# Kernel optimization log

Hardware: AMD Instinct MI355X
Metric: run time of the kernel (lower is better)

The kernel has to match this reference:

```python
import jax, jax.numpy as jnp
import numpy as np

# Finance / model constants (from Hyperparams)
S0 = 1.0
MU = 0.0
VOL = 0.2
TEXP = 5.0
PRINCIPAL = 100.0
LAM = 0.01
DT = 1.0 / 12.0
N_STEPS = 60            # texp / dt
GMDB = 100.0            # gmdb_frac * principal
FEE = 0.0196            # stand-in for analytics.calc_fair_fee(...)
BATCH = 65536
HIDDEN = 128
W_STD = 0.05
B_STD = 0.05


def setup_inputs() -> dict:
    key = jax.random.key(0)
    ks = jax.random.split(key, 8)
    # GBM paths: spots[i, j] = spot at time index i on path j, shape [N_STEPS+1, BATCH]
    z = jax.random.normal(ks[0], (N_STEPS, BATCH), dtype=jnp.float32)
    logret = (MU - 0.5 * VOL * VOL) * DT + VOL * np.sqrt(DT).astype(np.float32) * z
    spots = S0 * jnp.exp(jnp.concatenate([jnp.zeros((1, BATCH), jnp.float32),
                                          jnp.cumsum(logret, axis=0)], axis=0))
    tn = lambda k, shape, std: (jax.random.truncated_normal(k, -2.0, 2.0, shape, jnp.float32) * std)
    return {
        "spots": spots,
        "W1": tn(ks[1], (2, HIDDEN), W_STD),
        "b1": tn(ks[2], (HIDDEN,), B_STD),
        "W2": tn(ks[3], (HIDDEN, HIDDEN), W_STD),
        "b2": tn(ks[4], (HIDDEN,), B_STD),
        "W3": tn(ks[5], (HIDDEN, 1), W_STD),
        "b3": tn(ks[6], (1,), B_STD),
    }


def _hedge_delta(x, W1, b1, W2, b2, W3, b3):
    # 2-hidden-layer ReLU MLP -> 1 output; hedge delta = -(net(x))^2
    h = jax.nn.relu(x @ W1 + b1)
    h = jax.nn.relu(h @ W2 + b2)
    out = h @ W3 + b3          # [B, 1]
    return -(out ** 2)[:, 0]   # [B]


def reference(spots, W1, b1, W2, b2, W3, b3):
    """compute_pnl: returns per-path integrated PNL, shape [BATCH]."""
    ts = jnp.arange(N_STEPS, dtype=spots.dtype) * DT  # [N_STEPS]

    def step(pnl, xs):
        spot, spot_next, t = xs  # spot: [B]
        inputs = jnp.stack([spot, spot * 0 + t], axis=1)  # [B, 2]
        delta = _hedge_delta(inputs, W1, b1, W2, b2, W3, b3)
        delta = delta * jnp.minimum(jnp.exp(-0.01 * delta), 1.0)
        delta = delta * ((1.0 - jnp.exp(-LAM * (TEXP - t))) * PRINCIPAL)
        account = PRINCIPAL * spot / S0 * jnp.exp(-FEE * t)
        fee = FEE * DT * account * jnp.exp(-LAM * t)
        payout = LAM * DT * jnp.maximum(GMDB - account, 0.0) * jnp.exp(-LAM * t)
        inc_pnl = fee - payout
        pnl = pnl + inc_pnl + delta * (spot_next - spot)
        return pnl, None

    pnl0 = jnp.zeros(spots.shape[1], dtype=spots.dtype)
    pnl, _ = jax.lax.scan(step, pnl0, (spots[:-1], spots[1:], ts))
    return pnl
```

## Files before the change

### kernel.cpp

```cpp
#include <hip/hip_runtime.h>
#include <math.h>

namespace {
constexpr int kBatch = 65536;
constexpr int kSteps = 60;
constexpr int kNodes = 256;
constexpr float kInvDx = 16.0f;
constexpr float kDx    = 1.0f / 16.0f;

constexpr int kTPS   = kNodes / 16;
constexpr int kTiles = kSteps * kTPS;
constexpr int kBuildBlocks = 480;

constexpr float kDT        = 1.0f / 12.0f;
constexpr float kLam       = 0.01f;
constexpr float kTexp      = 5.0f;
constexpr float kPrincipal = 100.0f;
constexpr float kGmdb      = 100.0f;
constexpr float kFee       = 0.0196f;
}

typedef short short8 __attribute__((ext_vector_type(8)));
typedef float f32x4  __attribute__((ext_vector_type(4)));

__device__ inline short f2bf(float f) {
    unsigned u = __builtin_bit_cast(unsigned, f);
    u += 0x7FFFu + ((u >> 16) & 1u);
    return (short)(u >> 16);
}

__device__ inline unsigned short f2h_bits(float f) {
    return __builtin_bit_cast(unsigned short, (_Float16)f);
}
__device__ inline float h2f(unsigned short h) {
    return (float)__builtin_bit_cast(_Float16, h);
}

__global__ __launch_bounds__(256) void va_build_table(
    const float* __restrict__ W1,
    const float* __restrict__ b1,
    const float* __restrict__ W2,
    const float* __restrict__ b2,
    const float* __restrict__ W3,
    const float* __restrict__ b3,
    unsigned* __restrict__ tabu)
{
    const int tid   = threadIdx.x;
    const int lane  = tid & 63;
    const int lo    = lane & 15;
    const int hi    = lane >> 4;
    const int wv    = tid >> 6;
    const int mslot = wv >> 1;
    const int nh    = wv & 1;

    short8 bfrag[4][4];
    float  b2v[4], w3v[4];
    #pragma unroll
    for (int nt = 0; nt < 4; ++nt) {
        const int col = nh * 64 + nt * 16 + lo;
        b2v[nt] = b2[col];
        w3v[nt] = W3[col];
        #pragma unroll
        for (int kc = 0; kc < 4; ++kc) {
            const int kb = kc * 32 + hi * 8;
            short8 bf;
            #pragma unroll
            for (int e = 0; e < 8; ++e)
                bf[e] = f2bf(W2[(kb + e) * 128 + col]);
            bfrag[nt][kc] = bf;
        }
    }
    const float b3v = b3[0];

    __shared__ float red[2][2][16][4];

    for (int tile = blockIdx.x * 2 + mslot; tile < kTiles;
         tile += 2 * kBuildBlocks) {
        const int   s    = tile / kTPS;
        const int   n0   = (tile % kTPS) * 16;
        const float t    = (float)s * kDT;
        const float spot = (float)(n0 + lo) * kDx;

        short8 afrag[4];
        #pragma unroll
        for (int kc = 0; kc < 4; ++kc) {
            const int kb = kc * 32 + hi * 8;
            const f32x4* aw = reinterpret_cast<const f32x4*>(W1 + kb);
            const f32x4* ap = reinterpret_cast<const f32x4*>(W1 + 128 + kb);
            const f32x4* ab = reinterpret_cast<const f32x4*>(b1 + kb);
            const f32x4 a0 = aw[0], a1 = aw[1];
            const f32x4 p0 = ap[0], p1 = ap[1];
            const f32x4 c0 = ab[0], c1 = ab[1];
            short8 af;
            #pragma unroll
            for (int e = 0; e < 4; ++e) {
                float h = fmaxf(fmaf(spot, a0[e], fmaf(t, p0[e], c0[e])), 0.0f);
                af[e] = f2bf(h);
            }
            #pragma unroll
            for (int e = 0; e < 4; ++e) {
                float h = fmaxf(fmaf(spot, a1[e], fmaf(t, p1[e], c1[e])), 0.0f);
                af[4 + e] = f2bf(h);
            }
            afrag[kc] = af;
        }

        f32x4 acc[4];
        #pragma unroll
        for (int nt = 0; nt < 4; ++nt) {
            f32x4 a = {b2v[nt], b2v[nt], b2v[nt], b2v[nt]};
            #pragma unroll
            for (int kc = 0; kc < 4; ++kc)
                a = __builtin_amdgcn_mfma_f32_16x16x32_bf16(afrag[kc], bfrag[nt][kc], a, 0, 0, 0);
            acc[nt] = a;
        }

        float part[4];
        #pragma unroll
        for (int r = 0; r < 4; ++r) {
            float p = 0.0f;
            #pragma unroll
            for (int nt = 0; nt < 4; ++nt)
                p = fmaf(fmaxf(acc[nt][r], 0.0f), w3v[nt], p);
            part[r] = p;
        }
        #pragma unroll
        for (int m = 1; m < 16; m <<= 1) {
            #pragma unroll
            for (int r = 0; r < 4; ++r)
                part[r] += __shfl_xor(part[r], m);
        }
        if (lo == 0) {
            #pragma unroll
            for (int r = 0; r < 4; ++r)
                red[mslot][nh][hi][r] = part[r];
        }
        __syncthreads();

        if (tid < 32) {
            const int ms  = tid >> 4;
            const int idx = tid & 15;
            const int tms = (int)(blockIdx.x * 2 + ms)
                          + (tile - (int)(blockIdx.x * 2 + mslot));
            const int   ss   = tms / kTPS;
            const int   nn   = (tms % kTPS) * 16 + idx;
            const float tt   = (float)ss * kDT;
            const float spn  = (float)nn * kDx;
            const float outv = b3v + red[ms][0][idx >> 2][idx & 3]
                                   + red[ms][1][idx >> 2][idx & 3];

            float delta = -(outv * outv);
            delta *= fminf(expf(-0.01f * delta), 1.0f);
            delta *= (1.0f - expf(-kLam * (kTexp - tt))) * kPrincipal;

            const float elt     = expf(-kLam * tt);
            const float account = kPrincipal * spn * expf(-kFee * tt);
            const float fee     = kFee * kDT * account * elt;
            const float payout  = kLam * kDT * fmaxf(kGmdb - account, 0.0f) * elt;

            const unsigned pair = (unsigned)f2h_bits(delta)
                                | ((unsigned)f2h_bits(fee - payout) << 16);
            const int idx2 = 2 * (ss * kNodes + nn);
            tabu[idx2] = pair;
            if (nn > 0) tabu[idx2 - 1] = pair;
        }
        __syncthreads();
    }
}

__global__ __launch_bounds__(256) void va_main_kernel(
    const float* __restrict__ spots,
    const unsigned* __restrict__ tabu,
    float* __restrict__ out)
{
    const int lane = threadIdx.x & 63;
    const int wv   = threadIdx.x >> 6;
    const int pair = blockIdx.x * 64 + lane;
    const int s0   = wv * 15;

    float2 sp[16];
    #pragma unroll
    for (int k = 0; k < 16; ++k)
        sp[k] = *reinterpret_cast<const float2*>(spots + (s0 + k) * kBatch + 2 * pair);

    float pnl0 = 0.0f, pnl1 = 0.0f;
    #pragma unroll
    for (int k = 0; k < 15; ++k) {
        {
            const float x = sp[k].x * kInvDx;
            int i = (int)x;
            i = i > kNodes - 2 ? kNodes - 2 : i;
            const float fr = x - (float)i;
            const uint2 e = *reinterpret_cast<const uint2*>(
                tabu + 2 * ((s0 + k) * kNodes + i));
            const float d0 = h2f((unsigned short)(e.x & 0xFFFFu));
            const float f0 = h2f((unsigned short)(e.x >> 16));
            const float d1 = h2f((unsigned short)(e.y & 0xFFFFu));
            const float f1 = h2f((unsigned short)(e.y >> 16));
            pnl0 += fmaf(fr, f1 - f0, f0)
                  + fmaf(fr, d1 - d0, d0) * (sp[k + 1].x - sp[k].x);
        }
        {
            const float x = sp[k].y * kInvDx;
            int i = (int)x;
            i = i > kNodes - 2 ? kNodes - 2 : i;
            const float fr = x - (float)i;
            const uint2 e = *reinterpret_cast<const uint2*>(
                tabu + 2 * ((s0 + k) * kNodes + i));
            const float d0 = h2f((unsigned short)(e.x & 0xFFFFu));
            const float f0 = h2f((unsigned short)(e.x >> 16));
            const float d1 = h2f((unsigned short)(e.y & 0xFFFFu));
            const float f1 = h2f((unsigned short)(e.y >> 16));
            pnl1 += fmaf(fr, f1 - f0, f0)
                  + fmaf(fr, d1 - d0, d0) * (sp[k + 1].y - sp[k].y);
        }
    }

    __shared__ float2 red[256];
    red[threadIdx.x] = make_float2(pnl0, pnl1);
    __syncthreads();

    if (threadIdx.x < 64) {
        const float2 a = red[lane],       b = red[64 + lane];
        const float2 c = red[128 + lane], d = red[192 + lane];
        const float2 r = make_float2((a.x + b.x) + (c.x + d.x),
                                     (a.y + b.y) + (c.y + d.y));
        *reinterpret_cast<float2*>(out + blockIdx.x * 128 + 2 * lane) = r;
    }
}

extern "C" void kernel_launch(void* const* d_in, const int* in_sizes, int n_in,
                              void* d_out, int out_size, void* d_ws, size_t ws_size,
                              hipStream_t stream)
{
    const float* spots = (const float*)d_in[0];
    const float* W1    = (const float*)d_in[1];
    const float* b1    = (const float*)d_in[2];
    const float* W2    = (const float*)d_in[3];
    const float* b2    = (const float*)d_in[4];
    const float* W3    = (const float*)d_in[5];
    const float* b3    = (const float*)d_in[6];
    float* out = (float*)d_out;
    unsigned* tabu = (unsigned*)d_ws;

    va_build_table<<<kBuildBlocks, dim3(256), 0, stream>>>(
        W1, b1, W2, b2, W3, b3, tabu);
    va_main_kernel<<<kBatch / 128, dim3(256), 0, stream>>>(spots, tabu, out);
}
```

Baseline: 16.34 us.

## Stage compact interpolation table in LDS instead of gathering duplicated pairs

The build kernel now writes each table node once instead of storing duplicated neighbour pairs, halving the table size. The main kernel copies the whole 60-step table (about 60 KB) into shared memory per block, then does its two-node interpolation lookups from LDS. This is meant to replace scattered global/L2 gathers with cheap LDS reads. In exchange, every block re-reads the full table from L2, and the large LDS footprint limits how many blocks can run per CU.

New measurement: 16.61 us. About the same (+1.6%).

```diff
diff --git a/kernel.cpp b/kernel.cpp
--- a/kernel.cpp
+++ b/kernel.cpp
@@ -11,6 +11,8 @@
 constexpr int kTPS   = kNodes / 16;
 constexpr int kTiles = kSteps * kTPS;
 constexpr int kBuildBlocks = 480;
+
+constexpr int kTabUints = kSteps * kNodes;
 
 constexpr float kDT        = 1.0f / 12.0f;
 constexpr float kLam       = 0.01f;
@@ -158,11 +160,8 @@
             const float fee     = kFee * kDT * account * elt;
             const float payout  = kLam * kDT * fmaxf(kGmdb - account, 0.0f) * elt;
 
-            const unsigned pair = (unsigned)f2h_bits(delta)
-                                | ((unsigned)f2h_bits(fee - payout) << 16);
-            const int idx2 = 2 * (ss * kNodes + nn);
-            tabu[idx2] = pair;
-            if (nn > 0) tabu[idx2 - 1] = pair;
+            tabu[ss * kNodes + nn] = (unsigned)f2h_bits(delta)
+                                   | ((unsigned)f2h_bits(fee - payout) << 16);
         }
         __syncthreads();
     }
@@ -178,25 +177,37 @@
     const int pair = blockIdx.x * 64 + lane;
     const int s0   = wv * 15;
 
+    __shared__ unsigned tabs[kTabUints];
+
     float2 sp[16];
     #pragma unroll
     for (int k = 0; k < 16; ++k)
         sp[k] = *reinterpret_cast<const float2*>(spots + (s0 + k) * kBatch + 2 * pair);
 
+    {
+        const uint4* src = reinterpret_cast<const uint4*>(tabu);
+        uint4*       dst = reinterpret_cast<uint4*>(tabs);
+        #pragma unroll
+        for (int i = 0; i < 15; ++i)
+            dst[threadIdx.x + i * 256] = src[threadIdx.x + i * 256];
+    }
+    __syncthreads();
+
     float pnl0 = 0.0f, pnl1 = 0.0f;
     #pragma unroll
     for (int k = 0; k < 15; ++k) {
+        const int base = (s0 + k) * kNodes;
         {
             const float x = sp[k].x * kInvDx;
             int i = (int)x;
             i = i > kNodes - 2 ? kNodes - 2 : i;
             const float fr = x - (float)i;
-            const uint2 e = *reinterpret_cast<const uint2*>(
-                tabu + 2 * ((s0 + k) * kNodes + i));
-            const float d0 = h2f((unsigned short)(e.x & 0xFFFFu));
-            const float f0 = h2f((unsigned short)(e.x >> 16));
-            const float d1 = h2f((unsigned short)(e.y & 0xFFFFu));
-            const float f1 = h2f((unsigned short)(e.y >> 16));
+            const unsigned e0 = tabs[base + i];
+            const unsigned e1 = tabs[base + i + 1];
+            const float d0 = h2f((unsigned short)(e0 & 0xFFFFu));
+            const float f0 = h2f((unsigned short)(e0 >> 16));
+            const float d1 = h2f((unsigned short)(e1 & 0xFFFFu));
+            const float f1 = h2f((unsigned short)(e1 >> 16));
             pnl0 += fmaf(fr, f1 - f0, f0)
                   + fmaf(fr, d1 - d0, d0) * (sp[k + 1].x - sp[k].x);
         }
@@ -205,17 +216,18 @@
             int i = (int)x;
             i = i > kNodes - 2 ? kNodes - 2 : i;
             const float fr = x - (float)i;
-            const uint2 e = *reinterpret_cast<const uint2*>(
-                tabu + 2 * ((s0 + k) * kNodes + i));
-            const float d0 = h2f((unsigned short)(e.x & 0xFFFFu));
-            const float f0 = h2f((unsigned short)(e.x >> 16));
-            const float d1 = h2f((unsigned short)(e.y & 0xFFFFu));
-            const float f1 = h2f((unsigned short)(e.y >> 16));
+            const unsigned e0 = tabs[base + i];
+            const unsigned e1 = tabs[base + i + 1];
+            const float d0 = h2f((unsigned short)(e0 & 0xFFFFu));
+            const float f0 = h2f((unsigned short)(e0 >> 16));
+            const float d1 = h2f((unsigned short)(e1 & 0xFFFFu));
+            const float f1 = h2f((unsigned short)(e1 >> 16));
             pnl1 += fmaf(fr, f1 - f0, f0)
                   + fmaf(fr, d1 - d0, d0) * (sp[k + 1].y - sp[k].y);
         }
     }
 
+    __syncthreads();
     __shared__ float2 red[256];
     red[threadIdx.x] = make_float2(pnl0, pnl1);
     __syncthreads();
```
